# Optimization experiments

Hardware: AMD Instinct MI355X
Metric: run time of the kernel (lower is better)

Reference implementation:

```python
import jax, jax.numpy as jnp
import numpy as np

ALPHA = 0.2      # leak / integration time constant
E_FRAC = 0.8     # fraction of excitatory units (Dale's law)
NUM_LAYERS = 3


def setup_inputs() -> dict:
    key = jax.random.key(0)
    T, B, IN, H = 128, 64, 512, 1024
    ks = jax.random.split(key, 7)
    inputs = jax.random.normal(ks[0], (T, B, IN), jnp.float32)
    hidden_init = jax.random.uniform(ks[1], (1, B, H), jnp.float32) * 0.1
    # positive weights (clamped-positive in the original EI cell); Dale sign applied in reference
    W_in0 = jax.random.uniform(ks[2], (H, IN), jnp.float32) * (1.0 / np.sqrt(IN))
    W_in1 = jax.random.uniform(ks[3], (H, H), jnp.float32) * (1.0 / np.sqrt(H))
    W_in2 = jax.random.uniform(ks[4], (H, H), jnp.float32) * (1.0 / np.sqrt(H))
    W_rec = jax.random.uniform(ks[5], (NUM_LAYERS, H, H), jnp.float32) * (1.0 / H)
    b = jnp.zeros((NUM_LAYERS, H), jnp.float32)
    return {"inputs": inputs, "hidden_init": hidden_init, "W_in0": W_in0,
            "W_in1": W_in1, "W_in2": W_in2, "W_rec": W_rec, "b": b}


def reference(inputs, hidden_init, W_in0, W_in1, W_in2, W_rec, b):
    H = W_rec.shape[-1]
    ne = int(H * E_FRAC)
    signs = jnp.concatenate([jnp.ones((ne,), inputs.dtype), -jnp.ones((H - ne,), inputs.dtype)])
    e_mask = (signs > 0).astype(inputs.dtype)           # [H], zero out inhibitory feedforward
    # Dale's law: positive magnitudes with fixed presynaptic sign (columns)
    W_eff = jnp.abs(W_rec) * signs[None, None, :]        # [L, H, H]
    W_ins = (jnp.abs(W_in0), jnp.abs(W_in1), jnp.abs(W_in2))
    h0 = hidden_init[0]                                  # [B, H], shared across layers

    def step(carry, x_t):
        hs, vs = carry
        cell_input = x_t
        new_hs, new_vs = [], []
        for j in range(NUM_LAYERS):
            pre = cell_input @ W_ins[j].T + hs[j] @ W_eff[j].T + b[j]
            v = (1.0 - ALPHA) * vs[j] + ALPHA * pre      # leaky preact state
            h = jax.nn.relu(v)
            cell_input = h * e_mask                      # only excitatory units project forward
            new_hs.append(h)
            new_vs.append(v)
        return (tuple(new_hs), tuple(new_vs)), (cell_input, jnp.stack(new_hs))

    init = (tuple(h0 for _ in range(NUM_LAYERS)),
            tuple(jnp.zeros_like(h0) for _ in range(NUM_LAYERS)))
    _, (outputs, hiddens) = jax.lax.scan(step, init, inputs)
    # outputs: [T, B, H]; hiddens: [T, L, B, H] -> per-layer [T+1, B, H] incl. init
    hiddens = jnp.moveaxis(hiddens, 1, 0)                # [L, T, B, H]
    init_stack = jnp.broadcast_to(h0, (NUM_LAYERS, 1) + h0.shape)
    all_hiddens = jnp.concatenate([init_stack, hiddens], axis=1)  # [L, T+1, B, H]
    return outputs, all_hiddens
```

## Files before the change

kernel.cpp:

```cpp
#include <hip/hip_runtime.h>

#define T_STEPS 128
#define BATCH   64
#define INDIM   512
#define HDIM    1024
#define NE      819
#define OUT0_SZ (T_STEPS*BATCH*HDIM)
#define BH      (BATCH*HDIM)
#define ALLH_L  (129*BH)

#define HS_LAY   131072
#define HS_SLOT  393216
#define NSLOT    131
#define XF_T     65536
#define NBLK     192
#define NGRP     8
#define GSZ      24

typedef short bf16x8 __attribute__((ext_vector_type(8)));
typedef short short2v __attribute__((ext_vector_type(2)));
typedef float f32x4  __attribute__((ext_vector_type(4)));
typedef float f32x2  __attribute__((ext_vector_type(2)));

__device__ __forceinline__ short f2bf(float f){
    unsigned u = __float_as_uint(f);
    u += 0x7FFF + ((u >> 16) & 1);
    return (short)(u >> 16);
}
__device__ __forceinline__ float bf2f(short s){
    return __uint_as_float(((unsigned)(unsigned short)s) << 16);
}

__global__ __launch_bounds__(256) void ei_prep_w(const float* __restrict__ Win0,
        const float* __restrict__ Win1, const float* __restrict__ Win2,
        const float* __restrict__ Wrec, short* __restrict__ wf){
    int gid = blockIdx.x * 256 + threadIdx.x;
    int j, local, nkb, kff; const float* Win; short* base;
    if (gid < 196608)      { j=0; local=gid;        nkb=48; kff=512;  Win=Win0; base=wf; }
    else if (gid < 458752) { j=1; local=gid-196608; nkb=64; kff=1024; Win=Win1; base=wf+3145728; }
    else                   { j=2; local=gid-458752; nkb=64; kff=1024; Win=Win2; base=wf+7340032; }
    int lane = local & 63;
    int fi   = local >> 6;
    int kb   = fi % nkb;
    int it   = fi / nkb;
    int i    = it*16 + (lane & 15);
    int k0   = kb*32 + ((lane >> 4) << 3);
    const float* wrec_row = Wrec + ((size_t)j*HDIM + i)*HDIM;
    bf16x8 hv, lv;
    #pragma unroll
    for (int e = 0; e < 8; ++e){
        int k = k0 + e;
        float w;
        if (k < kff){
            w = fabsf(Win[(size_t)i*kff + k]);
            if (j != 0 && k >= NE) w = 0.f;
        } else {
            int kr = k - kff;
            w = fabsf(wrec_row[kr]);
            if (kr >= NE) w = -w;
        }
        short h = f2bf(w);
        hv[e] = h;
        lv[e] = f2bf(w - bf2f(h));
    }
    short* dst = base + (size_t)fi*1024 + lane*8;
    *(bf16x8*)dst         = hv;
    *(bf16x8*)(dst + 512) = lv;
}

__global__ __launch_bounds__(256) void ei_prep_xf(const float* __restrict__ x,
        short* __restrict__ xf){
    int gid = blockIdx.x * 256 + threadIdx.x;
    int lane = gid & 63;
    int bt   = (gid >> 6) & 3;
    int kb   = (gid >> 8) & 15;
    int t    = gid >> 12;
    int b = bt*16 + (lane & 15);
    int k = kb*32 + ((lane >> 4) << 3);
    const float* src = x + ((size_t)t*BATCH + b)*INDIM + k;
    float4 v0 = *(const float4*)src;
    float4 v1 = *(const float4*)(src + 4);
    float f[8] = {v0.x,v0.y,v0.z,v0.w,v1.x,v1.y,v1.z,v1.w};
    bf16x8 hv, lv;
    #pragma unroll
    for (int e = 0; e < 8; ++e){
        short h = f2bf(f[e]);
        hv[e] = h; lv[e] = f2bf(f[e] - bf2f(h));
    }
    short* dst = xf + (size_t)t*XF_T + (((size_t)(kb*4 + bt)) << 9) + lane*8;
    *(bf16x8*)dst            = hv;
    *(bf16x8*)(dst + 32768)  = lv;
}

__global__ __launch_bounds__(256) void ei_init5(const float* __restrict__ h0,
        float* __restrict__ out, short* __restrict__ hf, int* __restrict__ bar){
    int idx = blockIdx.x * 256 + threadIdx.x;
    int l = idx >> 16, r = idx & 0xFFFF;
    out[OUT0_SZ + (size_t)l*ALLH_L + r] = h0[r];
    if (idx < 1024) bar[idx] = 0;
    if (idx < 24576){
        int lane = idx & 63, bt = (idx >> 6) & 3, kb = (idx >> 8) & 31, j = idx >> 13;
        int b = bt*16 + (lane & 15);
        int k = kb*32 + ((lane >> 4) << 3);
        const float* src = h0 + (size_t)b*HDIM + k;
        float4 v0 = *(const float4*)src;
        float4 v1 = *(const float4*)(src + 4);
        float f[8] = {v0.x,v0.y,v0.z,v0.w,v1.x,v1.y,v1.z,v1.w};
        bf16x8 hv, lv;
        #pragma unroll
        for (int e = 0; e < 8; ++e){
            short hh = f2bf(f[e]);
            hv[e] = hh; lv[e] = f2bf(f[e] - bf2f(hh));
        }
        int off = ((kb*4 + bt) << 9) + lane*8;
        short* b0 = hf + (size_t)j*HS_LAY + off;
        *(bf16x8*)b0           = hv;
        *(bf16x8*)(b0 + 65536) = lv;
    }
}

template<int NKW, int NKFF, int FFLO>
__device__ __forceinline__ void step_mm2(
        const short* __restrict__ pff, const short* __restrict__ prec,
        const short* __restrict__ wp0, const short* __restrict__ wp1,
        int kb0, int btbase, int laneo, f32x4 acc[2][2])
{
    bf16x8 wh[2][2], wl[2][2], ah[2][2], al[2][2];
    auto loadW = [&](int kk, int buf){
        const short* a = wp0 + ((kb0 + kk) << 10);
        const short* b = wp1 + ((kb0 + kk) << 10);
        wh[buf][0] = *(const bf16x8*)a; wl[buf][0] = *(const bf16x8*)(a + 512);
        wh[buf][1] = *(const bf16x8*)b; wl[buf][1] = *(const bf16x8*)(b + 512);
    };
    auto loadA = [&](int kk, int buf){
        int kb = kb0 + kk;
        const short* pa; int lo;
        if (kb < NKFF){ pa = pff + (kb << 11); lo = FFLO; }
        else          { pa = prec + ((kb - NKFF) << 11); lo = 65536; }
        ah[buf][0] = *(const bf16x8*)(pa + ((btbase + 0) << 9) + laneo);
        ah[buf][1] = *(const bf16x8*)(pa + ((btbase + 1) << 9) + laneo);
        al[buf][0] = *(const bf16x8*)(pa + lo + ((btbase + 0) << 9) + laneo);
        al[buf][1] = *(const bf16x8*)(pa + lo + ((btbase + 1) << 9) + laneo);
    };
    loadW(0, 0); loadA(0, 0);
    #pragma unroll
    for (int kk = 0; kk < NKW; ++kk){
        if (kk + 1 < NKW){ loadW(kk + 1, (kk + 1) & 1); loadA(kk + 1, (kk + 1) & 1); }
        const int b = kk & 1;
        acc[0][0] = __builtin_amdgcn_mfma_f32_16x16x32_bf16(ah[b][0], wh[b][0], acc[0][0], 0,0,0);
        acc[0][1] = __builtin_amdgcn_mfma_f32_16x16x32_bf16(ah[b][1], wh[b][0], acc[0][1], 0,0,0);
        acc[1][0] = __builtin_amdgcn_mfma_f32_16x16x32_bf16(ah[b][0], wh[b][1], acc[1][0], 0,0,0);
        acc[1][1] = __builtin_amdgcn_mfma_f32_16x16x32_bf16(ah[b][1], wh[b][1], acc[1][1], 0,0,0);
        acc[0][0] = __builtin_amdgcn_mfma_f32_16x16x32_bf16(al[b][0], wh[b][0], acc[0][0], 0,0,0);
        acc[0][1] = __builtin_amdgcn_mfma_f32_16x16x32_bf16(al[b][1], wh[b][0], acc[0][1], 0,0,0);
        acc[1][0] = __builtin_amdgcn_mfma_f32_16x16x32_bf16(al[b][0], wh[b][1], acc[1][0], 0,0,0);
        acc[1][1] = __builtin_amdgcn_mfma_f32_16x16x32_bf16(al[b][1], wh[b][1], acc[1][1], 0,0,0);
        acc[0][0] = __builtin_amdgcn_mfma_f32_16x16x32_bf16(ah[b][0], wl[b][0], acc[0][0], 0,0,0);
        acc[0][1] = __builtin_amdgcn_mfma_f32_16x16x32_bf16(ah[b][1], wl[b][0], acc[0][1], 0,0,0);
        acc[1][0] = __builtin_amdgcn_mfma_f32_16x16x32_bf16(ah[b][0], wl[b][1], acc[1][0], 0,0,0);
        acc[1][1] = __builtin_amdgcn_mfma_f32_16x16x32_bf16(ah[b][1], wl[b][1], acc[1][1], 0,0,0);
    }
}

__global__ __launch_bounds__(512, 2) void ei_persist3(
        const short* __restrict__ xf, const short* __restrict__ wf,
        const float* __restrict__ bias, float* __restrict__ out,
        short* __restrict__ hf, int* __restrict__ bar)
{
    const int bid   = blockIdx.x;
    const int g     = bid & 7;
    const int w     = bid >> 3;
    const int j     = w >> 3;
    const int strip = g*4 + ((w >> 1) & 3);
    const int bhalf = w & 1;
    const int grp   = g;

    const int tx    = threadIdx.x;
    const int wv    = tx >> 6, lane = tx & 63;
    const int laneo = lane * 8;
    const int btbase = bhalf * 2;
    const int it0   = strip * 2;

    const short* wfj = wf + (j == 0 ? 0 : (j == 1 ? 3145728 : 7340032));
    const int nkb  = (j == 0) ? 48 : 64;
    const int NKW  = nkb >> 3;
    const int kb0  = wv * NKW;
    const short* wp0 = wfj + it0*nkb*1024 + laneo;
    const short* wp1 = wp0 + nkb*1024;

    const int bl  = tx >> 4;
    const int il0 = (tx & 15) << 1;
    const int i_g = strip*32 + il0;
    const int b_g = bhalf*32 + bl;
    const f32x2 bb = *(const f32x2*)&bias[j*HDIM + i_g];
    f32x2 vreg = {0.f, 0.f};

    const int kb4 = i_g >> 5, btw = b_g >> 4;
    const int lnw = (b_g & 15) + (((i_g >> 3) & 3) << 4);
    const int hoff = ((kb4*4 + btw) << 9) + lnw*8 + (i_g & 7);

    __shared__ float psum[8][32][34];

    for (int s = 0; s < T_STEPS + 2; ++s){
        const int t = s - j;
        const bool act = (t >= 0) && (t < T_STEPS);
        if (act){
            const short* hfr  = hf + (size_t)s*HS_SLOT;
            const short* prec = (t == 0) ? (hf + (size_t)j*HS_LAY)
                                         : (hfr + (size_t)j*HS_LAY);
            f32x4 acc[2][2] = {{{0.f,0.f,0.f,0.f},{0.f,0.f,0.f,0.f}},
                               {{0.f,0.f,0.f,0.f},{0.f,0.f,0.f,0.f}}};
            if (j == 0)
                step_mm2<6,16,32768>(xf + (size_t)t*XF_T, prec, wp0, wp1, kb0, btbase, laneo, acc);
            else if (j == 1)
                step_mm2<8,32,65536>(hfr, prec, wp0, wp1, kb0, btbase, laneo, acc);
            else
                step_mm2<8,32,65536>(hfr + HS_LAY, prec, wp0, wp1, kb0, btbase, laneo, acc);

            const int r0 = (lane >> 4) << 2, l15 = lane & 15;
            #pragma unroll
            for (int ic = 0; ic < 2; ++ic)
                #pragma unroll
                for (int bt = 0; bt < 2; ++bt)
                    #pragma unroll
                    for (int r = 0; r < 4; ++r)
                        psum[wv][bt*16 + r0 + r][ic*16 + l15] = acc[ic][bt][r];
        }
        __syncthreads();
        if (act){
            float sum0 = 0.f, sum1 = 0.f;
            #pragma unroll
            for (int ww = 0; ww < 8; ++ww){
                f32x2 p = *(f32x2*)&psum[ww][bl][il0];
                sum0 += p[0]; sum1 += p[1];
            }
            vreg[0] = 0.8f*vreg[0] + 0.2f*(sum0 + bb[0]);
            vreg[1] = 0.8f*vreg[1] + 0.2f*(sum1 + bb[1]);
            float h0v = vreg[0] > 0.f ? vreg[0] : 0.f;
            float h1v = vreg[1] > 0.f ? vreg[1] : 0.f;
            f32x2 hv2 = {h0v, h1v};
            *(f32x2*)&out[OUT0_SZ + ((size_t)(j*129 + t + 1))*BH + b_g*HDIM + i_g] = hv2;
            short hh0 = f2bf(h0v), hl0 = f2bf(h0v - bf2f(hh0));
            short hh1 = f2bf(h1v), hl1 = f2bf(h1v - bf2f(hh1));
            int hi2 = (int)(unsigned short)hh0 | ((int)(unsigned short)hh1 << 16);
            int lo2 = (int)(unsigned short)hl0 | ((int)(unsigned short)hl1 << 16);
            short* hww = hf + (size_t)(s + 1)*HS_SLOT + (size_t)j*HS_LAY + hoff;
            asm volatile("global_store_dword %0, %1, off sc0 sc1"
                         :: "v"(hww), "v"(hi2) : "memory");
            asm volatile("global_store_dword %0, %1, off sc0 sc1"
                         :: "v"(hww + 65536), "v"(lo2) : "memory");
            if (j == 2){
                f32x2 o2 = {(i_g < NE) ? h0v : 0.f, (i_g + 1 < NE) ? h1v : 0.f};
                *(f32x2*)&out[(size_t)t*BH + b_g*HDIM + i_g] = o2;
            }
        }
        if (s == T_STEPS + 1) break;
        asm volatile("s_waitcnt vmcnt(0)" ::: "memory");
        __syncthreads();
        if (tx == 0){
            int prev = __hip_atomic_fetch_add(&bar[grp*32], 1,
                        __ATOMIC_RELAXED, __HIP_MEMORY_SCOPE_AGENT);
            if (prev == (s + 1)*GSZ - 1){
                int sp = __hip_atomic_fetch_add(&bar[256], 1,
                        __ATOMIC_RELAXED, __HIP_MEMORY_SCOPE_AGENT);
                if (sp == (s + 1)*NGRP - 1){
                    #pragma unroll
                    for (int gg = 0; gg < NGRP; ++gg)
                        __hip_atomic_store(&bar[512 + gg*32], s + 1,
                                __ATOMIC_RELAXED, __HIP_MEMORY_SCOPE_AGENT);
                }
            }
            while (__hip_atomic_load(&bar[512 + grp*32],
                    __ATOMIC_RELAXED, __HIP_MEMORY_SCOPE_AGENT) < s + 1)
                __builtin_amdgcn_s_sleep(2);
        }
        __syncthreads();
    }
}

#define HS_PAR_FB 393216
__global__ __launch_bounds__(256) void ei_init3(const float* __restrict__ h0,
        float* __restrict__ out, float* __restrict__ v_ws, short* __restrict__ hfb){
    int idx = blockIdx.x * 256 + threadIdx.x;
    int l = idx >> 16, r = idx & 0xFFFF;
    float h = h0[r];
    out[OUT0_SZ + (size_t)l*ALLH_L + r] = h;
    v_ws[idx] = 0.f;
    if (idx < 24576){
        int lane = idx & 63, bt = (idx >> 6) & 3, kb = (idx >> 8) & 31, j = idx >> 13;
        int b = bt*16 + (lane & 15);
        int k = kb*32 + ((lane >> 4) << 3);
        const float* src = h0 + (size_t)b*HDIM + k;
        float4 v0 = *(const float4*)src;
        float4 v1 = *(const float4*)(src + 4);
        float f[8] = {v0.x,v0.y,v0.z,v0.w,v1.x,v1.y,v1.z,v1.w};
        bf16x8 hv, lv;
        #pragma unroll
        for (int e = 0; e < 8; ++e){
            short hh = f2bf(f[e]);
            hv[e] = hh; lv[e] = f2bf(f[e] - bf2f(hh));
        }
        int off = ((kb*4 + bt) << 9) + lane*8;
        short* b0 = hfb + (size_t)j*HS_LAY + off;
        *(bf16x8*)b0           = hv;
        *(bf16x8*)(b0 + 65536) = lv;
        short* b1 = b0 + HS_PAR_FB;
        *(bf16x8*)b1           = hv;
        *(bf16x8*)(b1 + 65536) = lv;
    }
}

template<int NKW, int NKFF, int FFLO>
__device__ __forceinline__ void stage_body5(
        const short* __restrict__ pff, const short* __restrict__ prec,
        const short* __restrict__ wp, int kb0, int laneo, f32x4 acc[4])
{
    bf16x8 wbh[NKW], wbl[NKW];
    #pragma unroll
    for (int kk = 0; kk < NKW; ++kk){
        const short* w0 = wp + ((kb0 + kk) << 10);
        wbh[kk] = *(const bf16x8*)w0;
        wbl[kk] = *(const bf16x8*)(w0 + 512);
    }
    bf16x8 ah[2][4], al[2][4];
    auto loadA = [&](int kk, int buf){
        int kb = kb0 + kk;
        const short* pa; int lo;
        if (kb < NKFF){ pa = pff + (kb << 11); lo = FFLO; }
        else          { pa = prec + ((kb - NKFF) << 11); lo = 65536; }
        #pragma unroll
        for (int bt = 0; bt < 4; ++bt){
            ah[buf][bt] = *(const bf16x8*)(pa + (bt << 9) + laneo);
            al[buf][bt] = *(const bf16x8*)(pa + lo + (bt << 9) + laneo);
        }
    };
    loadA(0, 0);
    #pragma unroll
    for (int kk = 0; kk < NKW; ++kk){
        if (kk + 1 < NKW) loadA(kk + 1, (kk + 1) & 1);
        const int bf = kk & 1;
        #pragma unroll
        for (int bt = 0; bt < 4; ++bt)
            acc[bt] = __builtin_amdgcn_mfma_f32_16x16x32_bf16(ah[bf][bt], wbh[kk], acc[bt], 0,0,0);
        #pragma unroll
        for (int bt = 0; bt < 4; ++bt)
            acc[bt] = __builtin_amdgcn_mfma_f32_16x16x32_bf16(al[bf][bt], wbh[kk], acc[bt], 0,0,0);
        #pragma unroll
        for (int bt = 0; bt < 4; ++bt)
            acc[bt] = __builtin_amdgcn_mfma_f32_16x16x32_bf16(ah[bf][bt], wbl[kk], acc[bt], 0,0,0);
    }
}

__global__ __launch_bounds__(512, 2) void ei_stage5(
        const short* __restrict__ xf, const short* __restrict__ wf,
        const float* __restrict__ bias, float* __restrict__ out,
        float* __restrict__ v_ws, short* __restrict__ hfb, int s)
{
    int j = blockIdx.x >> 6;
    int t = s - j;
    if (t < 0 || t >= T_STEPS) return;
    int it = blockIdx.x & 63;
    int wv = threadIdx.x >> 6, lane = threadIdx.x & 63;
    int laneo = lane * 8;
    int par_r = (s - 1) & 1, par_w = s & 1;
    const short* hfr  = hfb + par_r*HS_PAR_FB;
    const short* prec = hfr + j*HS_LAY;

    f32x4 acc[4] = {{0.f,0.f,0.f,0.f},{0.f,0.f,0.f,0.f},
                    {0.f,0.f,0.f,0.f},{0.f,0.f,0.f,0.f}};

    if (j == 0){
        const short* pff = xf + t*XF_T;
        const short* wp  = wf + it*48*1024 + laneo;
        stage_body5<6,16,32768>(pff, prec, wp, wv*6, laneo, acc);
    } else if (j == 1){
        const short* pff = hfr;
        const short* wp  = wf + 3145728 + it*64*1024 + laneo;
        stage_body5<8,32,65536>(pff, prec, wp, wv*8, laneo, acc);
    } else {
        const short* pff = hfr + HS_LAY;
        const short* wp  = wf + 7340032 + it*64*1024 + laneo;
        stage_body5<8,32,65536>(pff, prec, wp, wv*8, laneo, acc);
    }

    __shared__ float psum[8][64][18];
    {
        int r0 = (lane >> 4) << 2, l15 = lane & 15;
        #pragma unroll
        for (int bt = 0; bt < 4; ++bt)
            #pragma unroll
            for (int r = 0; r < 4; ++r)
                psum[wv][bt*16 + r0 + r][l15] = acc[bt][r];
    }
    __syncthreads();

    int tx  = threadIdx.x;
    int b   = tx >> 3;
    int il0 = (tx & 7) << 1;
    float* allh = out + OUT0_SZ + ((size_t)(j*129 + t + 1))*BH;
    float* outp = out + (size_t)t*BH;
    short* hww  = hfb + par_w*HS_PAR_FB + j*HS_LAY;
    float sum0 = 0.f, sum1 = 0.f;
    #pragma unroll
    for (int w = 0; w < 8; ++w){
        f32x2 p = *(f32x2*)&psum[w][b][il0];
        sum0 += p[0]; sum1 += p[1];
    }
    int i = it*16 + il0;
    f32x2 bb = *(const f32x2*)&bias[j*HDIM + i];
    int vo = (j*BATCH + b)*HDIM + i;
    f32x2 vold = *(f32x2*)&v_ws[vo];
    float vn0 = 0.8f * vold[0] + 0.2f * (sum0 + bb[0]);
    float vn1 = 0.8f * vold[1] + 0.2f * (sum1 + bb[1]);
    f32x2 vnv = {vn0, vn1};
    *(f32x2*)&v_ws[vo] = vnv;
    float h0 = vn0 > 0.f ? vn0 : 0.f;
    float h1 = vn1 > 0.f ? vn1 : 0.f;
    f32x2 hv2 = {h0, h1};
    *(f32x2*)&allh[b*HDIM + i] = hv2;
    short hh0 = f2bf(h0), hl0 = f2bf(h0 - bf2f(hh0));
    short hh1 = f2bf(h1), hl1 = f2bf(h1 - bf2f(hh1));
    int kb  = i >> 5, btw = b >> 4;
    int lnw = (b & 15) + (((i >> 3) & 3) << 4);
    int off = ((kb*4 + btw) << 9) + lnw*8 + (i & 7);
    short2v hi2 = {hh0, hh1}, lo2 = {hl0, hl1};
    *(short2v*)(hww + off)         = hi2;
    *(short2v*)(hww + off + 65536) = lo2;
    if (j == 2){
        f32x2 o2 = {(i < NE) ? h0 : 0.f, (i + 1 < NE) ? h1 : 0.f};
        *(f32x2*)&outp[b*HDIM + i] = o2;
    }
}

extern "C" void kernel_launch(void* const* d_in, const int* in_sizes, int n_in,
                              void* d_out, int out_size, void* d_ws, size_t ws_size,
                              hipStream_t stream) {
    const float* xin  = (const float*)d_in[0];
    const float* h0   = (const float*)d_in[1];
    const float* Win0 = (const float*)d_in[2];
    const float* Win1 = (const float*)d_in[3];
    const float* Win2 = (const float*)d_in[4];
    const float* Wrec = (const float*)d_in[5];
    const float* bias = (const float*)d_in[6];
    float* out  = (float*)d_out;
    char* ws    = (char*)d_ws;

    const size_t HF_B   = (size_t)NSLOT * HS_SLOT * 2ULL;
    const size_t need_p = 4096 + HF_B + 16777216ULL + 23068672ULL;
    const size_t need_f = 786432ULL + 1572864ULL + 16777216ULL + 23068672ULL;

    if (ws_size >= need_p) {
        int*   bar = (int*)ws;
        short* hf  = (short*)(ws + 4096);
        short* xf  = (short*)(ws + 4096 + HF_B);
        short* wfp = (short*)(ws + 4096 + HF_B + 16777216ULL);
        hipLaunchKernelGGL(ei_prep_w, dim3(2816), dim3(256), 0, stream,
                           Win0, Win1, Win2, Wrec, wfp);
        hipLaunchKernelGGL(ei_prep_xf, dim3(2048), dim3(256), 0, stream, xin, xf);
        hipLaunchKernelGGL(ei_init5, dim3(768), dim3(256), 0, stream, h0, out, hf, bar);
        hipLaunchKernelGGL(ei_persist3, dim3(NBLK), dim3(512), 0, stream,
                           xf, wfp, bias, out, hf, bar);
    } else {
        float* v_ws = (float*)ws;
        short* hfb  = (short*)(ws + 786432);
        short* xf   = (short*)(ws + 786432 + 1572864ULL);
        short* wfp  = (short*)(ws + 786432 + 1572864ULL + 16777216ULL);
        hipLaunchKernelGGL(ei_prep_w, dim3(2816), dim3(256), 0, stream,
                           Win0, Win1, Win2, Wrec, wfp);
        hipLaunchKernelGGL(ei_prep_xf, dim3(2048), dim3(256), 0, stream, xin, xf);
        hipLaunchKernelGGL(ei_init3, dim3(768), dim3(256), 0, stream, h0, out, v_ws, hfb);
        for (int s = 0; s < T_STEPS + 2; ++s)
            hipLaunchKernelGGL(ei_stage5, dim3(192), dim3(512), 0, stream,
                               xf, wfp, bias, out, v_ws, hfb, s);
    }
}
```

Measured before the change: 1.079 ms.

## Prefetch all activation fragments upfront and remap epilogue threads for coalesced stores

The step GEMM now issues every activation (hi/lo bf16) load for the wave's K range before the MFMA loop, keeping only the weights double-buffered. This is meant to hide the latency of the freshly written hidden-state reads behind one batch of loads. The epilogue thread mapping is changed so each thread's hidden-state store offset is contiguous in the packed layout, and the layer-2 output store is moved ahead of the bf16 stores. The barrier spin sleep is shortened and the barrier region in the workspace is enlarged. Holding all activation fragments in registers raises VGPR pressure under the 512x2 launch bound.

```diff
diff --git a/kernel.cpp b/kernel.cpp
--- a/kernel.cpp
+++ b/kernel.cpp
@@ -120,49 +120,56 @@
 }
 
 template<int NKW, int NKFF, int FFLO>
-__device__ __forceinline__ void step_mm2(
+__device__ __forceinline__ void step_mm3(
         const short* __restrict__ pff, const short* __restrict__ prec,
         const short* __restrict__ wp0, const short* __restrict__ wp1,
         int kb0, int btbase, int laneo, f32x4 acc[2][2])
 {
-    bf16x8 wh[2][2], wl[2][2], ah[2][2], al[2][2];
-    auto loadW = [&](int kk, int buf){
-        const short* a = wp0 + ((kb0 + kk) << 10);
-        const short* b = wp1 + ((kb0 + kk) << 10);
-        wh[buf][0] = *(const bf16x8*)a; wl[buf][0] = *(const bf16x8*)(a + 512);
-        wh[buf][1] = *(const bf16x8*)b; wl[buf][1] = *(const bf16x8*)(b + 512);
-    };
-    auto loadA = [&](int kk, int buf){
+    bf16x8 ah[NKW][2], al[NKW][2];
+    #pragma unroll
+    for (int kk = 0; kk < NKW; ++kk){
         int kb = kb0 + kk;
         const short* pa; int lo;
         if (kb < NKFF){ pa = pff + (kb << 11); lo = FFLO; }
         else          { pa = prec + ((kb - NKFF) << 11); lo = 65536; }
-        ah[buf][0] = *(const bf16x8*)(pa + ((btbase + 0) << 9) + laneo);
-        ah[buf][1] = *(const bf16x8*)(pa + ((btbase + 1) << 9) + laneo);
-        al[buf][0] = *(const bf16x8*)(pa + lo + ((btbase + 0) << 9) + laneo);
-        al[buf][1] = *(const bf16x8*)(pa + lo + ((btbase + 1) << 9) + laneo);
-    };
-    loadW(0, 0); loadA(0, 0);
+        ah[kk][0] = *(const bf16x8*)(pa + ((btbase + 0) << 9) + laneo);
+        ah[kk][1] = *(const bf16x8*)(pa + ((btbase + 1) << 9) + laneo);
+        al[kk][0] = *(const bf16x8*)(pa + lo + ((btbase + 0) << 9) + laneo);
+        al[kk][1] = *(const bf16x8*)(pa + lo + ((btbase + 1) << 9) + laneo);
+    }
+    bf16x8 wh[2][2], wl[2][2];
+    {
+        const short* a = wp0 + (kb0 << 10);
+        const short* b = wp1 + (kb0 << 10);
+        wh[0][0] = *(const bf16x8*)a; wl[0][0] = *(const bf16x8*)(a + 512);
+        wh[0][1] = *(const bf16x8*)b; wl[0][1] = *(const bf16x8*)(b + 512);
+    }
     #pragma unroll
     for (int kk = 0; kk < NKW; ++kk){
-        if (kk + 1 < NKW){ loadW(kk + 1, (kk + 1) & 1); loadA(kk + 1, (kk + 1) & 1); }
-        const int b = kk & 1;
-        acc[0][0] = __builtin_amdgcn_mfma_f32_16x16x32_bf16(ah[b][0], wh[b][0], acc[0][0], 0,0,0);
-        acc[0][1] = __builtin_amdgcn_mfma_f32_16x16x32_bf16(ah[b][1], wh[b][0], acc[0][1], 0,0,0);
-        acc[1][0] = __builtin_amdgcn_mfma_f32_16x16x32_bf16(ah[b][0], wh[b][1], acc[1][0], 0,0,0);
-        acc[1][1] = __builtin_amdgcn_mfma_f32_16x16x32_bf16(ah[b][1], wh[b][1], acc[1][1], 0,0,0);
-        acc[0][0] = __builtin_amdgcn_mfma_f32_16x16x32_bf16(al[b][0], wh[b][0], acc[0][0], 0,0,0);
-        acc[0][1] = __builtin_amdgcn_mfma_f32_16x16x32_bf16(al[b][1], wh[b][0], acc[0][1], 0,0,0);
-        acc[1][0] = __builtin_amdgcn_mfma_f32_16x16x32_bf16(al[b][0], wh[b][1], acc[1][0], 0,0,0);
-        acc[1][1] = __builtin_amdgcn_mfma_f32_16x16x32_bf16(al[b][1], wh[b][1], acc[1][1], 0,0,0);
-        acc[0][0] = __builtin_amdgcn_mfma_f32_16x16x32_bf16(ah[b][0], wl[b][0], acc[0][0], 0,0,0);
-        acc[0][1] = __builtin_amdgcn_mfma_f32_16x16x32_bf16(ah[b][1], wl[b][0], acc[0][1], 0,0,0);
-        acc[1][0] = __builtin_amdgcn_mfma_f32_16x16x32_bf16(ah[b][0], wl[b][1], acc[1][0], 0,0,0);
-        acc[1][1] = __builtin_amdgcn_mfma_f32_16x16x32_bf16(ah[b][1], wl[b][1], acc[1][1], 0,0,0);
-    }
-}
-
-__global__ __launch_bounds__(512, 2) void ei_persist3(
+        if (kk + 1 < NKW){
+            const int nb = (kk + 1) & 1;
+            const short* a = wp0 + ((kb0 + kk + 1) << 10);
+            const short* b = wp1 + ((kb0 + kk + 1) << 10);
+            wh[nb][0] = *(const bf16x8*)a; wl[nb][0] = *(const bf16x8*)(a + 512);
+            wh[nb][1] = *(const bf16x8*)b; wl[nb][1] = *(const bf16x8*)(b + 512);
+        }
+        const int b2 = kk & 1;
+        acc[0][0] = __builtin_amdgcn_mfma_f32_16x16x32_bf16(ah[kk][0], wh[b2][0], acc[0][0], 0,0,0);
+        acc[0][1] = __builtin_amdgcn_mfma_f32_16x16x32_bf16(ah[kk][1], wh[b2][0], acc[0][1], 0,0,0);
+        acc[1][0] = __builtin_amdgcn_mfma_f32_16x16x32_bf16(ah[kk][0], wh[b2][1], acc[1][0], 0,0,0);
+        acc[1][1] = __builtin_amdgcn_mfma_f32_16x16x32_bf16(ah[kk][1], wh[b2][1], acc[1][1], 0,0,0);
+        acc[0][0] = __builtin_amdgcn_mfma_f32_16x16x32_bf16(al[kk][0], wh[b2][0], acc[0][0], 0,0,0);
+        acc[0][1] = __builtin_amdgcn_mfma_f32_16x16x32_bf16(al[kk][1], wh[b2][0], acc[0][1], 0,0,0);
+        acc[1][0] = __builtin_amdgcn_mfma_f32_16x16x32_bf16(al[kk][0], wh[b2][1], acc[1][0], 0,0,0);
+        acc[1][1] = __builtin_amdgcn_mfma_f32_16x16x32_bf16(al[kk][1], wh[b2][1], acc[1][1], 0,0,0);
+        acc[0][0] = __builtin_amdgcn_mfma_f32_16x16x32_bf16(ah[kk][0], wl[b2][0], acc[0][0], 0,0,0);
+        acc[0][1] = __builtin_amdgcn_mfma_f32_16x16x32_bf16(ah[kk][1], wl[b2][0], acc[0][1], 0,0,0);
+        acc[1][0] = __builtin_amdgcn_mfma_f32_16x16x32_bf16(ah[kk][0], wl[b2][1], acc[1][0], 0,0,0);
+        acc[1][1] = __builtin_amdgcn_mfma_f32_16x16x32_bf16(ah[kk][1], wl[b2][1], acc[1][1], 0,0,0);
+    }
+}
+
+__global__ __launch_bounds__(512, 2) void ei_persist5(
         const short* __restrict__ xf, const short* __restrict__ wf,
         const float* __restrict__ bias, float* __restrict__ out,
         short* __restrict__ hf, int* __restrict__ bar)
@@ -188,16 +195,17 @@
     const short* wp0 = wfj + it0*nkb*1024 + laneo;
     const short* wp1 = wp0 + nkb*1024;
 
-    const int bl  = tx >> 4;
-    const int il0 = (tx & 15) << 1;
-    const int i_g = strip*32 + il0;
-    const int b_g = bhalf*32 + bl;
+    const int btl = tx >> 8;
+    const int q   = tx & 255;
+    const int lnw = q >> 2;
+    const int e0  = (q & 3) * 2;
+    const int b_g = (bhalf*2 + btl)*16 + (lnw & 15);
+    const int i_g = strip*32 + ((lnw >> 4) << 3) + e0;
+    const int bl  = b_g & 31;
+    const int il0 = ((lnw >> 4) << 3) + e0;
+    const int hoff = ((strip*4 + bhalf*2 + btl) << 9) + q*2;
     const f32x2 bb = *(const f32x2*)&bias[j*HDIM + i_g];
     f32x2 vreg = {0.f, 0.f};
-
-    const int kb4 = i_g >> 5, btw = b_g >> 4;
-    const int lnw = (b_g & 15) + (((i_g >> 3) & 3) << 4);
-    const int hoff = ((kb4*4 + btw) << 9) + lnw*8 + (i_g & 7);
 
     __shared__ float psum[8][32][34];
 
@@ -211,11 +219,11 @@
             f32x4 acc[2][2] = {{{0.f,0.f,0.f,0.f},{0.f,0.f,0.f,0.f}},
                                {{0.f,0.f,0.f,0.f},{0.f,0.f,0.f,0.f}}};
             if (j == 0)
-                step_mm2<6,16,32768>(xf + (size_t)t*XF_T, prec, wp0, wp1, kb0, btbase, laneo, acc);
+                step_mm3<6,16,32768>(xf + (size_t)t*XF_T, prec, wp0, wp1, kb0, btbase, laneo, acc);
             else if (j == 1)
-                step_mm2<8,32,65536>(hfr, prec, wp0, wp1, kb0, btbase, laneo, acc);
+                step_mm3<8,32,65536>(hfr, prec, wp0, wp1, kb0, btbase, laneo, acc);
             else
-                step_mm2<8,32,65536>(hfr + HS_LAY, prec, wp0, wp1, kb0, btbase, laneo, acc);
+                step_mm3<8,32,65536>(hfr + HS_LAY, prec, wp0, wp1, kb0, btbase, laneo, acc);
 
             const int r0 = (lane >> 4) << 2, l15 = lane & 15;
             #pragma unroll
@@ -240,6 +248,10 @@
             float h1v = vreg[1] > 0.f ? vreg[1] : 0.f;
             f32x2 hv2 = {h0v, h1v};
             *(f32x2*)&out[OUT0_SZ + ((size_t)(j*129 + t + 1))*BH + b_g*HDIM + i_g] = hv2;
+            if (j == 2){
+                f32x2 o2 = {(i_g < NE) ? h0v : 0.f, (i_g + 1 < NE) ? h1v : 0.f};
+                *(f32x2*)&out[(size_t)t*BH + b_g*HDIM + i_g] = o2;
+            }
             short hh0 = f2bf(h0v), hl0 = f2bf(h0v - bf2f(hh0));
             short hh1 = f2bf(h1v), hl1 = f2bf(h1v - bf2f(hh1));
             int hi2 = (int)(unsigned short)hh0 | ((int)(unsigned short)hh1 << 16);
@@ -249,10 +261,6 @@
                          :: "v"(hww), "v"(hi2) : "memory");
             asm volatile("global_store_dword %0, %1, off sc0 sc1"
                          :: "v"(hww + 65536), "v"(lo2) : "memory");
-            if (j == 2){
-                f32x2 o2 = {(i_g < NE) ? h0v : 0.f, (i_g + 1 < NE) ? h1v : 0.f};
-                *(f32x2*)&out[(size_t)t*BH + b_g*HDIM + i_g] = o2;
-            }
         }
         if (s == T_STEPS + 1) break;
         asm volatile("s_waitcnt vmcnt(0)" ::: "memory");
@@ -272,7 +280,7 @@
             }
             while (__hip_atomic_load(&bar[512 + grp*32],
                     __ATOMIC_RELAXED, __HIP_MEMORY_SCOPE_AGENT) < s + 1)
-                __builtin_amdgcn_s_sleep(2);
+                __builtin_amdgcn_s_sleep(1);
         }
         __syncthreads();
     }
@@ -446,19 +454,18 @@
     char* ws    = (char*)d_ws;
 
     const size_t HF_B   = (size_t)NSLOT * HS_SLOT * 2ULL;
-    const size_t need_p = 4096 + HF_B + 16777216ULL + 23068672ULL;
-    const size_t need_f = 786432ULL + 1572864ULL + 16777216ULL + 23068672ULL;
+    const size_t need_p = 65536 + HF_B + 16777216ULL + 23068672ULL;
 
     if (ws_size >= need_p) {
         int*   bar = (int*)ws;
-        short* hf  = (short*)(ws + 4096);
-        short* xf  = (short*)(ws + 4096 + HF_B);
-        short* wfp = (short*)(ws + 4096 + HF_B + 16777216ULL);
+        short* hf  = (short*)(ws + 65536);
+        short* xf  = (short*)(ws + 65536 + HF_B);
+        short* wfp = (short*)(ws + 65536 + HF_B + 16777216ULL);
         hipLaunchKernelGGL(ei_prep_w, dim3(2816), dim3(256), 0, stream,
                            Win0, Win1, Win2, Wrec, wfp);
         hipLaunchKernelGGL(ei_prep_xf, dim3(2048), dim3(256), 0, stream, xin, xf);
         hipLaunchKernelGGL(ei_init5, dim3(768), dim3(256), 0, stream, h0, out, hf, bar);
-        hipLaunchKernelGGL(ei_persist3, dim3(NBLK), dim3(512), 0, stream,
+        hipLaunchKernelGGL(ei_persist5, dim3(NBLK), dim3(512), 0, stream,
                            xf, wfp, bias, out, hf, bar);
     } else {
         float* v_ws = (float*)ws;
```

After: 1.209 ms. +12.0%, slower.
